# Performance work log

Hardware: AMD Instinct MI355X
Metric: run time of the kernel (lower is better)

Reference implementation:

```python
import jax, jax.numpy as jnp
import numpy as np

N, E, G, H = 100000, 1600000, 256, 2
EPS = 1e-5


def _gat_conv(x, src, dst, W, a_src, a_dst, bias, C):
    # PyG GATConv (concat=True, negative_slope=0.2): lin has no bias, bias added after concat.
    h = (x @ W).reshape(N, H, C)                                   # [N,H,C]
    e_src = (h * a_src).sum(-1)                                    # [N,H]
    e_dst = (h * a_dst).sum(-1)                                    # [N,H]
    alpha = jax.nn.leaky_relu(e_src[src] + e_dst[dst], 0.2)        # [Etot,H]
    amax = jax.ops.segment_max(alpha, dst, num_segments=N)         # segment softmax over incoming edges
    ex = jnp.exp(alpha - amax[dst])
    denom = jax.ops.segment_sum(ex, dst, num_segments=N)
    msg = h[src] * ex[:, :, None]                                  # [Etot,H,C]
    out = jax.ops.segment_sum(msg, dst, num_segments=N) / (denom[:, :, None] + 1e-16)
    return out.reshape(N, H * C) + bias


def _bn(x, g, b, m, v):  # BatchNorm in eval mode with running stats
    return g * (x - m) * jax.lax.rsqrt(v + EPS) + b


def _forward(edge_index, batch, x, w1, as1, ad1, b1, g1, be1, m1, v1, p1w, p1b,
             w2, as2, ad2, b2, g2, be2, m2, v2, p2w, p2b,
             w3, as3, ad3, b3, g3, be3, m3, v3, p3w, p3b,
             fw, fb, g4, be4, m4, v4, l1w, l1b, l2w, l2b):
    loops = jnp.arange(N, dtype=edge_index.dtype)                  # GATConv add_self_loops=True
    src = jnp.concatenate([edge_index[0], loops])
    dst = jnp.concatenate([edge_index[1], loops])
    h = jax.nn.relu(_bn(_gat_conv(x, src, dst, w1, as1, ad1, b1, 32), g1, be1, m1, v1)) + (x @ p1w + p1b)
    h = jax.nn.relu(_bn(_gat_conv(h, src, dst, w2, as2, ad2, b2, 64), g2, be2, m2, v2)) + (h @ p2w + p2b)
    h = jax.nn.relu(_bn(_gat_conv(h, src, dst, w3, as3, ad3, b3, 64), g3, be3, m3, v3)) + (h @ p3w + p3b)
    counts = jax.ops.segment_sum(jnp.ones((N,), h.dtype), batch, num_segments=G)
    pooled = jax.ops.segment_sum(h, batch, num_segments=G) / jnp.maximum(counts, 1.0)[:, None]  # [G,128]
    z = jax.nn.relu(_bn(pooled @ fw + fb, g4, be4, m4, v4))
    z = jax.nn.relu(z @ l1w + l1b)
    return z @ l2w + l2b                                           # [G,10]


def setup_inputs():
    key = jax.random.key(0)
    ks = jax.random.split(key, 48)
    it = iter(range(48))
    def rn(shape, s=0.1):
        return jax.random.normal(ks[next(it)], shape, jnp.float32) * s
    def bn_params(dim):  # gamma, beta, running_mean, running_var
        return (jax.random.uniform(ks[next(it)], (dim,), jnp.float32, 0.5, 1.5),
                rn((dim,)), rn((dim,)),
                jax.random.uniform(ks[next(it)], (dim,), jnp.float32, 0.5, 1.5))
    inp = {}
    inp["x"] = jax.random.normal(ks[next(it)], (N, 5), jnp.float32)
    inp["edge_index"] = jax.random.randint(ks[next(it)], (2, E), 0, N, jnp.int32)
    inp["batch"] = jnp.sort(jax.random.randint(ks[next(it)], (N,), 0, G, jnp.int32))
    inp["w1"], inp["as1"], inp["ad1"], inp["b1"] = rn((5, 64)), rn((H, 32)), rn((H, 32)), rn((64,))
    inp["g1"], inp["be1"], inp["m1"], inp["v1"] = bn_params(64)
    inp["p1w"], inp["p1b"] = rn((5, 64)), rn((64,))
    inp["w2"], inp["as2"], inp["ad2"], inp["b2"] = rn((64, 128)), rn((H, 64)), rn((H, 64)), rn((128,))
    inp["g2"], inp["be2"], inp["m2"], inp["v2"] = bn_params(128)
    inp["p2w"], inp["p2b"] = rn((64, 128)), rn((128,))
    inp["w3"], inp["as3"], inp["ad3"], inp["b3"] = rn((128, 128)), rn((H, 64)), rn((H, 64)), rn((128,))
    inp["g3"], inp["be3"], inp["m3"], inp["v3"] = bn_params(128)
    inp["p3w"], inp["p3b"] = rn((128, 128)), rn((128,))
    inp["fw"], inp["fb"] = rn((128, 32)), rn((32,))
    inp["g4"], inp["be4"], inp["m4"], inp["v4"] = bn_params(32)
    inp["l1w"], inp["l1b"] = rn((32, 32)), rn((32,))
    inp["l2w"], inp["l2b"] = rn((32, 10)), rn((10,))
    return inp


def reference(x, edge_index, batch, w1, as1, ad1, b1, g1, be1, m1, v1, p1w, p1b,
              w2, as2, ad2, b2, g2, be2, m2, v2, p2w, p2b,
              w3, as3, ad3, b3, g3, be3, m3, v3, p3w, p3b,
              fw, fb, g4, be4, m4, v4, l1w, l1b, l2w, l2b):
    return _forward(edge_index, batch, x, w1, as1, ad1, b1, g1, be1, m1, v1, p1w, p1b,
                    w2, as2, ad2, b2, g2, be2, m2, v2, p2w, p2b,
                    w3, as3, ad3, b3, g3, be3, m3, v3, p3w, p3b,
                    fw, fb, g4, be4, m4, v4, l1w, l1b, l2w, l2b)
```

## Files before the change

### kernel.cpp

```cpp
#include <hip/hip_runtime.h>
#include <hip/hip_bf16.h>
#include <hip/hip_fp16.h>

#define NN   100000
#define EE   1600000
#define ETOT (EE + NN)
#define GG   256
#define BNEPS 1e-5f
#define NBK  391
#define PADTOT (ETOT + NBK * 4096 + 64)
#define PSPLIT 16

typedef float floatx2 __attribute__((ext_vector_type(2)));
typedef short s16x8 __attribute__((ext_vector_type(8)));
typedef float f32x4v __attribute__((ext_vector_type(4)));

__device__ __forceinline__ unsigned short f2bf(float f) {
    unsigned u = __float_as_uint(f);
    unsigned r = u + 0x7FFF + ((u >> 16) & 1);
    return (unsigned short)(r >> 16);
}
__device__ __forceinline__ float bf2f(unsigned short b) {
    return __uint_as_float(((unsigned)b) << 16);
}
__device__ __forceinline__ floatx2 pkfma(floatx2 a, floatx2 b, floatx2 c) {
    return __builtin_elementwise_fma(a, b, c);
}


__global__ __launch_bounds__(256) void bucket_count_kernel(
    const int* __restrict__ ei, int* __restrict__ bucket_cnt)
{
    __shared__ int cnt[NBK];
    for (int i = threadIdx.x; i < NBK; i += 256) cnt[i] = 0;
    __syncthreads();
    int base = blockIdx.x * 8192;
    for (int k = threadIdx.x; k < 8192; k += 256) {
        int e = base + k;
        if (e < ETOT) {
            int dst = (e < EE) ? ei[EE + e] : (e - EE);
            atomicAdd(&cnt[dst >> 8], 1);
        }
    }
    __syncthreads();
    for (int i = threadIdx.x; i < NBK; i += 256)
        if (cnt[i]) atomicAdd(&bucket_cnt[i], cnt[i]);
}

__global__ __launch_bounds__(512) void bucket_scan_kernel(
    const int* __restrict__ bucket_cnt, int* __restrict__ bucket_base,
    int* __restrict__ gcursor, float* __restrict__ esrcs)
{
    __shared__ int s[512];
    int t = threadIdx.x;
    int v = (t < NBK) ? bucket_cnt[t] : 0;
    s[t] = v;
    __syncthreads();
    int x = v;
    for (int o = 1; o < 512; o <<= 1) {
        int y = (t >= o) ? s[t - o] : 0;
        __syncthreads();
        x += y;
        s[t] = x;
        __syncthreads();
    }
    if (t < NBK) { bucket_base[t] = x - v; gcursor[t] = x - v; }
    if (t == 0) {
        bucket_base[NBK] = ETOT;
        esrcs[2 * NN]     = __int_as_float(0xFF800000);
        esrcs[2 * NN + 1] = __int_as_float(0xFF800000);
    }
}

__global__ __launch_bounds__(256) void partition_kernel(
    const int* __restrict__ ei, int* __restrict__ gcursor, int* __restrict__ part)
{
    __shared__ int cnt[NBK];
    __shared__ int basel[NBK];
    for (int i = threadIdx.x; i < NBK; i += 256) cnt[i] = 0;
    __syncthreads();
    int base = blockIdx.x * 4096;
    for (int k = threadIdx.x; k < 4096; k += 256) {
        int e = base + k;
        if (e < ETOT) {
            int dst = (e < EE) ? ei[EE + e] : (e - EE);
            atomicAdd(&cnt[dst >> 8], 1);
        }
    }
    __syncthreads();
    for (int i = threadIdx.x; i < NBK; i += 256) {
        int c = cnt[i];
        basel[i] = c ? atomicAdd(&gcursor[i], c) : 0;
        cnt[i] = 0;
    }
    __syncthreads();
    for (int k = threadIdx.x; k < 4096; k += 256) {
        int e = base + k;
        if (e < ETOT) {
            int src, dst;
            if (e < EE) { src = ei[e]; dst = ei[EE + e]; }
            else        { src = e - EE; dst = e - EE; }
            int b = dst >> 8;
            int slot = atomicAdd(&cnt[b], 1);
            part[basel[b] + slot] = src | ((dst & 255) << 17);
        }
    }
}

__global__ __launch_bounds__(256) void csr_build_kernel(
    const int* __restrict__ part, const int* __restrict__ bucket_base,
    int* __restrict__ row2_start, int* __restrict__ row2_deg,
    int* __restrict__ csr2_src)
{
    __shared__ int degs[256];
    __shared__ int sc[256];
    __shared__ int cur[256];
    int b = blockIdx.x;
    int t = threadIdx.x;
    int beg = bucket_base[b], end = bucket_base[b + 1];
    int pbase = ((beg + 7) & ~7) + 4096 * b;
    degs[t] = 0;
    __syncthreads();
    for (int j = beg + t; j < end; j += 256)
        atomicAdd(&degs[(part[j] >> 17) & 255], 1);
    __syncthreads();
    int dg = degs[t];
    int pdeg = (dg + 7) & ~7;
    sc[t] = pdeg;
    __syncthreads();
    int x = pdeg;
    for (int o = 1; o < 256; o <<= 1) {
        int y = (t >= o) ? sc[t - o] : 0;
        __syncthreads();
        x += y;
        sc[t] = x;
        __syncthreads();
    }
    int start2 = pbase + (x - pdeg);
    int node = b * 256 + t;
    if (node < NN) { row2_start[node] = start2; row2_deg[node] = dg; }
    cur[t] = start2;
    __syncthreads();
    for (int j = beg + t; j < end; j += 256) {
        int pv = part[j];
        int pos = atomicAdd(&cur[(pv >> 17) & 255], 1);
        csr2_src[pos] = pv & 0x1FFFF;
    }
    for (int k = dg; k < pdeg; ++k) csr2_src[start2 + k] = NN;
}


template<int K>
__device__ __forceinline__ void prep_w_body(
    int unit, const float* __restrict__ W, const float* __restrict__ pw,
    short* __restrict__ wfrag)
{
    constexpr int KS = K / 32;
    int total = 16 * KS * 2 * 64;
    if (unit >= total) return;
    int lane = unit & 63;
    int rest = unit >> 6;
    int hilo = rest & 1;
    int fk = rest >> 1;
    int ks = fk % KS;
    int nt = fk / KS;
    int n = nt * 16 + (lane & 15);
    int k0 = ks * 32 + (lane >> 4) * 8;
    const float* src = (n < 128) ? (W + n) : (pw + (n - 128));
    s16x8 out;
#pragma unroll
    for (int j = 0; j < 8; ++j) {
        float wv = src[(size_t)(k0 + j) * 128];
        unsigned short hi = f2bf(wv);
        if (hilo == 0) {
            out[j] = (short)hi;
        } else {
            float fhi = __uint_as_float(((unsigned)hi) << 16);
            out[j] = (short)f2bf(wv - fhi);
        }
    }
    *(s16x8*)(wfrag + (size_t)unit * 8) = out;
}

__global__ __launch_bounds__(256) void prep_all_kernel(
    const float* __restrict__ w2, const float* __restrict__ p2w, short* __restrict__ wfrag2,
    const float* __restrict__ w3, const float* __restrict__ p3w, short* __restrict__ wfrag3,
    const float* b1, const float* g1, const float* be1, const float* m1, const float* v1,
    const float* b2, const float* g2, const float* be2, const float* m2, const float* v2,
    const float* b3, const float* g3, const float* be3, const float* m3, const float* v3,
    float* sc1, float* sh1, float* sc2, float* sh2, float* sc3, float* sh3)
{
    int b = blockIdx.x;
    int tid = threadIdx.x;
    if (b < 16) {
        prep_w_body<64>(b * 256 + tid, w2, p2w, wfrag2);
    } else if (b < 48) {
        prep_w_body<128>((b - 16) * 256 + tid, w3, p3w, wfrag3);
    } else {
        int t = tid;
        if (t < 128) {
            if (t < 64) {
                float sc = g1[t] * rsqrtf(v1[t] + BNEPS);
                sc1[t] = sc;
                sh1[t] = (b1[t] - m1[t]) * sc + be1[t];
            }
            {
                float sc = g2[t] * rsqrtf(v2[t] + BNEPS);
                sc2[t] = sc;
                sh2[t] = (b2[t] - m2[t]) * sc + be2[t];
            }
            {
                float sc = g3[t] * rsqrtf(v3[t] + BNEPS);
                sc3[t] = sc;
                sh3[t] = (b3[t] - m3[t]) * sc + be3[t];
            }
        }
    }
}


__global__ __launch_bounds__(256) void edgew_kernel(
    const int* __restrict__ csr2_src, const int* __restrict__ row2_start,
    const int* __restrict__ row2_deg,
    const float2* __restrict__ esrc, const float2* __restrict__ edst,
    unsigned* __restrict__ csr_w, int nN)
{
    int n = blockIdx.x * 8 + (threadIdx.x >> 5);
    int hl = threadIdx.x & 31;
    if (n >= nN) return;
    float2 ed = edst[n];
    int s2 = row2_start[n];
    int dg = row2_deg[n];
    int pc = (dg + 7) & ~7;
    for (int j = hl; j < pc; j += 32) {
        int i = csr2_src[s2 + j];
        float2 es = esrc[i];
        float a0 = es.x + ed.x; a0 = (a0 > 0.f) ? a0 : 0.2f * a0;
        float a1 = es.y + ed.y; a1 = (a1 > 0.f) ? a1 : 0.2f * a1;
        unsigned w = (unsigned)f2bf(__expf(a0)) | ((unsigned)f2bf(__expf(a1)) << 16);
        csr_w[s2 + j] = w;
    }
}


__global__ __launch_bounds__(256) void feat1_kernel(
    const float* __restrict__ xin, const float* __restrict__ W,
    const float* __restrict__ pw, const float* __restrict__ pb,
    const float* __restrict__ a_src, const float* __restrict__ a_dst,
    unsigned char* __restrict__ h8, float* __restrict__ esrc, float* __restrict__ edst,
    unsigned short* __restrict__ rout16, int nN)
{
    constexpr int F_IN = 5, F_OUT = 64;
    int t = threadIdx.x;
    int n = blockIdx.x * 4 + t / F_OUT;
    int f = t % F_OUT;
    if (n >= nN) return;
    float acc = 0.f, racc = 0.f;
#pragma unroll
    for (int k = 0; k < F_IN; ++k) {
        float xv = xin[n * F_IN + k];
        acc  += xv * W[k * F_OUT + f];
        racc += xv * pw[k * F_OUT + f];
    }
    float other = __shfl_xor(acc, 1, 64);
    if ((f & 1) == 0) {
        int p = __builtin_amdgcn_cvt_pk_fp8_f32(acc, other, 0, false);
        *(unsigned short*)(h8 + (size_t)n * F_OUT + f) = (unsigned short)(p & 0xFFFF);
    }
    rout16[(size_t)n * F_OUT + f] = f2bf(racc + pb[f]);
    float es = acc * a_src[f];
    float ed = acc * a_dst[f];
#pragma unroll
    for (int off = 16; off > 0; off >>= 1) {
        es += __shfl_xor(es, off, 32);
        ed += __shfl_xor(ed, off, 32);
    }
    if ((t & 31) == 0) {
        int head = (f >> 5) & 1;
        esrc[n * 2 + head] = es;
        edst[n * 2 + head] = ed;
    }
}


template<int K>
__global__ __launch_bounds__(512, 4) void mfma_feat_kernel(
    const unsigned short* __restrict__ xin16, const short* __restrict__ wfrag,
    const float* __restrict__ pb,
    const float* __restrict__ a_src, const float* __restrict__ a_dst,
    unsigned char* __restrict__ h8, float* __restrict__ esrc, float* __restrict__ edst,
    unsigned short* __restrict__ rout16)
{
    constexpr int KS = K / 32;
    constexpr int CH = K / 8;
    __shared__ __align__(16) char smem[1024 * CH + 28672];
    s16x8* xs = (s16x8*)smem;
    unsigned short* h8lds = (unsigned short*)(smem + 1024 * CH);
    unsigned short* rolds = (unsigned short*)(smem + 1024 * CH + 9216);
    float2* espart = (float2*)(smem + 1024 * CH + 26624);

    const int tid = threadIdx.x;
    const int base = blockIdx.x * 64;

    for (int idx = tid; idx < 64 * CH; idx += 512) {
        int node = idx / CH;
        int ch = idx % CH;
        int gn = base + node; if (gn > NN - 1) gn = NN - 1;
        s16x8 v = *(const s16x8*)(xin16 + (size_t)gn * K + ch * 8);
        int tt = node >> 4, mm = node & 15;
        xs[(tt * CH + ch) * 16 + mm] = v;
    }
    __syncthreads();

    const int w = tid >> 6;
    const int lane = tid & 63;
    const int quad = lane >> 4;
    const int m = lane & 15;
    const int nt0 = 2 * w, nt1 = nt0 + 1;

    s16x8 bA[2 * KS], bB[2 * KS];
#pragma unroll
    for (int i = 0; i < 2 * KS; ++i) {
        bA[i] = *(const s16x8*)(wfrag + (size_t)((nt0 * KS * 2 + i) * 64 + lane) * 8);
        bB[i] = *(const s16x8*)(wfrag + (size_t)((nt1 * KS * 2 + i) * 64 + lane) * 8);
    }

    const bool hpart = (w < 4);
    float av0 = 0.f, dv0 = 0.f, av1 = 0.f, dv1 = 0.f, bv0 = 0.f, bv1 = 0.f;
    if (hpart) {
        av0 = a_src[nt0 * 16 + m]; dv0 = a_dst[nt0 * 16 + m];
        av1 = a_src[nt1 * 16 + m]; dv1 = a_dst[nt1 * 16 + m];
    } else {
        bv0 = pb[(nt0 - 8) * 16 + m]; bv1 = pb[(nt1 - 8) * 16 + m];
    }

#pragma unroll
    for (int rt = 0; rt < 4; ++rt) {
        s16x8 a[KS];
#pragma unroll
        for (int ks = 0; ks < KS; ++ks)
            a[ks] = xs[(rt * CH + ks * 4 + quad) * 16 + m];
        f32x4v cA = {0.f, 0.f, 0.f, 0.f};
        f32x4v cB = {0.f, 0.f, 0.f, 0.f};
#pragma unroll
        for (int ks = 0; ks < KS; ++ks) {
            cA = __builtin_amdgcn_mfma_f32_16x16x32_bf16(a[ks], bA[2 * ks + 0], cA, 0, 0, 0);
            cA = __builtin_amdgcn_mfma_f32_16x16x32_bf16(a[ks], bA[2 * ks + 1], cA, 0, 0, 0);
            cB = __builtin_amdgcn_mfma_f32_16x16x32_bf16(a[ks], bB[2 * ks + 0], cB, 0, 0, 0);
            cB = __builtin_amdgcn_mfma_f32_16x16x32_bf16(a[ks], bB[2 * ks + 1], cB, 0, 0, 0);
        }
        int row0 = rt * 16 + quad * 4;
        if (hpart) {
#pragma unroll
            for (int r = 0; r < 4; ++r) {
                float v0 = cA[r], v1 = cB[r];
                float es = v0 * av0 + v1 * av1;
                float ed = v0 * dv0 + v1 * dv1;
#pragma unroll
                for (int off = 8; off > 0; off >>= 1) {
                    es += __shfl_xor(es, off, 16);
                    ed += __shfl_xor(ed, off, 16);
                }
                if (m == 0) espart[w * 64 + row0 + r] = make_float2(es, ed);
                float p0 = __shfl_xor(v0, 1, 16);
                float p1 = __shfl_xor(v1, 1, 16);
                if ((m & 1) == 0) {
                    int pk0 = __builtin_amdgcn_cvt_pk_fp8_f32(v0, p0, 0, false);
                    int pk1 = __builtin_amdgcn_cvt_pk_fp8_f32(v1, p1, 0, false);
                    h8lds[(row0 + r) * 72 + nt0 * 8 + (m >> 1)] = (unsigned short)(pk0 & 0xFFFF);
                    h8lds[(row0 + r) * 72 + nt1 * 8 + (m >> 1)] = (unsigned short)(pk1 & 0xFFFF);
                }
            }
        } else {
#pragma unroll
            for (int r = 0; r < 4; ++r) {
                rolds[(row0 + r) * 136 + (nt0 - 8) * 16 + m] = f2bf(cA[r] + bv0);
                rolds[(row0 + r) * 136 + (nt1 - 8) * 16 + m] = f2bf(cB[r] + bv1);
            }
        }
    }

    __syncthreads();

    if (tid < 64) {
        int node = base + tid;
        if (node < NN) {
            float2 e0 = espart[0 * 64 + tid];
            float2 e1 = espart[1 * 64 + tid];
            float2 e2 = espart[2 * 64 + tid];
            float2 e3 = espart[3 * 64 + tid];
            ((float2*)esrc)[node] = make_float2(e0.x + e1.x, e2.x + e3.x);
            ((float2*)edst)[node] = make_float2(e0.y + e1.y, e2.y + e3.y);
        }
    }
    for (int i = tid; i < 64 * 8; i += 512) {
        int row = i >> 3, ch = i & 7;
        int node = base + row;
        if (node < NN) {
            int4 v = *(const int4*)((char*)h8lds + row * 144 + ch * 16);
            *(int4*)(h8 + (size_t)node * 128 + ch * 16) = v;
        }
    }
    for (int i = tid; i < 64 * 16; i += 512) {
        int row = i >> 4, ch = i & 15;
        int node = base + row;
        if (node < NN) {
            int4 v = *(const int4*)((char*)rolds + row * 272 + ch * 16);
            *(int4*)((char*)rout16 + (size_t)node * 256 + ch * 16) = v;
        }
    }
}


__global__ __launch_bounds__(256) void aggregate128_kernel(
    const unsigned char* __restrict__ h8,
    const int* __restrict__ row2_start, const int* __restrict__ row2_deg,
    const int* __restrict__ csr2_src, const unsigned* __restrict__ csr_w,
    const float* __restrict__ bnsc, const float* __restrict__ bnsh,
    unsigned short* __restrict__ io16)
{
    int w = threadIdx.x >> 6;
    int lane = threadIdx.x & 63;
    int half = lane >> 5;
    int fl = lane & 31;
    unsigned shl = (fl >= 16) ? 0u : 16u;
    int n = blockIdx.x * 8 + w * 2 + half;
    int s2 = row2_start[n];
    int dg = row2_deg[n];
    int pc = (dg + 7) & ~7;
    const int4* sp = (const int4*)(csr2_src + s2);
    const uint4* wp = (const uint4*)(csr_w + s2);
    float sa = 0.f, sb = 0.f;
    floatx2 acc01a = {0.f, 0.f}, acc23a = {0.f, 0.f};
    floatx2 acc01b = {0.f, 0.f}, acc23b = {0.f, 0.f};
    for (int j = 0; j < pc; j += 8) {
        int4 ia = sp[(j >> 2) + 0];
        int4 ib = sp[(j >> 2) + 1];
        uint4 wa = wp[(j >> 2) + 0];
        uint4 wb = wp[(j >> 2) + 1];
        unsigned d0 = *(const unsigned*)(h8 + (size_t)ia.x * 128 + fl * 4);
        unsigned d1 = *(const unsigned*)(h8 + (size_t)ia.y * 128 + fl * 4);
        unsigned d2 = *(const unsigned*)(h8 + (size_t)ia.z * 128 + fl * 4);
        unsigned d3 = *(const unsigned*)(h8 + (size_t)ia.w * 128 + fl * 4);
        unsigned d4 = *(const unsigned*)(h8 + (size_t)ib.x * 128 + fl * 4);
        unsigned d5 = *(const unsigned*)(h8 + (size_t)ib.y * 128 + fl * 4);
        unsigned d6 = *(const unsigned*)(h8 + (size_t)ib.z * 128 + fl * 4);
        unsigned d7 = *(const unsigned*)(h8 + (size_t)ib.w * 128 + fl * 4);
        float g0 = __uint_as_float((wa.x << shl) & 0xFFFF0000u);
        float g1 = __uint_as_float((wa.y << shl) & 0xFFFF0000u);
        float g2 = __uint_as_float((wa.z << shl) & 0xFFFF0000u);
        float g3 = __uint_as_float((wa.w << shl) & 0xFFFF0000u);
        float g4 = __uint_as_float((wb.x << shl) & 0xFFFF0000u);
        float g5 = __uint_as_float((wb.y << shl) & 0xFFFF0000u);
        float g6 = __uint_as_float((wb.z << shl) & 0xFFFF0000u);
        float g7 = __uint_as_float((wb.w << shl) & 0xFFFF0000u);
        floatx2 gv0 = {g0, g0};
        floatx2 gv1 = {g1, g1};
        floatx2 gv2 = {g2, g2};
        floatx2 gv3 = {g3, g3};
        floatx2 gv4 = {g4, g4};
        floatx2 gv5 = {g5, g5};
        floatx2 gv6 = {g6, g6};
        floatx2 gv7 = {g7, g7};
        acc01a = pkfma(gv0, __builtin_amdgcn_cvt_pk_f32_fp8((int)d0, false), acc01a);
        acc23a = pkfma(gv0, __builtin_amdgcn_cvt_pk_f32_fp8((int)d0, true),  acc23a);
        acc01a = pkfma(gv1, __builtin_amdgcn_cvt_pk_f32_fp8((int)d1, false), acc01a);
        acc23a = pkfma(gv1, __builtin_amdgcn_cvt_pk_f32_fp8((int)d1, true),  acc23a);
        acc01a = pkfma(gv2, __builtin_amdgcn_cvt_pk_f32_fp8((int)d2, false), acc01a);
        acc23a = pkfma(gv2, __builtin_amdgcn_cvt_pk_f32_fp8((int)d2, true),  acc23a);
        acc01a = pkfma(gv3, __builtin_amdgcn_cvt_pk_f32_fp8((int)d3, false), acc01a);
        acc23a = pkfma(gv3, __builtin_amdgcn_cvt_pk_f32_fp8((int)d3, true),  acc23a);
        acc01b = pkfma(gv4, __builtin_amdgcn_cvt_pk_f32_fp8((int)d4, false), acc01b);
        acc23b = pkfma(gv4, __builtin_amdgcn_cvt_pk_f32_fp8((int)d4, true),  acc23b);
        acc01b = pkfma(gv5, __builtin_amdgcn_cvt_pk_f32_fp8((int)d5, false), acc01b);
        acc23b = pkfma(gv5, __builtin_amdgcn_cvt_pk_f32_fp8((int)d5, true),  acc23b);
        acc01b = pkfma(gv6, __builtin_amdgcn_cvt_pk_f32_fp8((int)d6, false), acc01b);
        acc23b = pkfma(gv6, __builtin_amdgcn_cvt_pk_f32_fp8((int)d6, true),  acc23b);
        acc01b = pkfma(gv7, __builtin_amdgcn_cvt_pk_f32_fp8((int)d7, false), acc01b);
        acc23b = pkfma(gv7, __builtin_amdgcn_cvt_pk_f32_fp8((int)d7, true),  acc23b);
        sa += ((g0 + g1) + (g2 + g3));
        sb += ((g4 + g5) + (g6 + g7));
    }
    floatx2 acc01 = acc01a + acc01b;
    floatx2 acc23 = acc23a + acc23b;
    float s = sa + sb;
    float inv = 1.f / (s + 1e-16f);
    int f0 = fl * 4;
    float4 sc = *(const float4*)(bnsc + f0);
    float4 sh = *(const float4*)(bnsh + f0);
    float o0 = fmaf(acc01.x * inv, sc.x, sh.x);
    float o1 = fmaf(acc01.y * inv, sc.y, sh.y);
    float o2 = fmaf(acc23.x * inv, sc.z, sh.z);
    float o3 = fmaf(acc23.y * inv, sc.w, sh.w);
    uint2* iop = (uint2*)(io16 + (size_t)n * 128 + f0);
    uint2 pu = *iop;
    float r0 = fmaxf(o0, 0.f) + __uint_as_float((pu.x & 0xFFFFu) << 16);
    float r1 = fmaxf(o1, 0.f) + __uint_as_float(pu.x & 0xFFFF0000u);
    float r2 = fmaxf(o2, 0.f) + __uint_as_float((pu.y & 0xFFFFu) << 16);
    float r3 = fmaxf(o3, 0.f) + __uint_as_float(pu.y & 0xFFFF0000u);
    uint2 ov;
    ov.x = (unsigned)f2bf(r0) | ((unsigned)f2bf(r1) << 16);
    ov.y = (unsigned)f2bf(r2) | ((unsigned)f2bf(r3) << 16);
    *iop = ov;
}


__global__ __launch_bounds__(256) void aggregate64_kernel(
    const unsigned char* __restrict__ h8,
    const int* __restrict__ row2_start, const int* __restrict__ row2_deg,
    const int* __restrict__ csr2_src, const unsigned* __restrict__ csr_w,
    const float* __restrict__ bnsc, const float* __restrict__ bnsh,
    unsigned short* __restrict__ io16)
{
    int w = threadIdx.x >> 6;
    int lane = threadIdx.x & 63;
    int half = lane >> 5;
    int hl = lane & 31;
    int q  = hl >> 4;
    int fl = hl & 15;
    unsigned shl = (fl >= 8) ? 0u : 16u;
    int n = blockIdx.x * 8 + w * 2 + half;
    int s2 = row2_start[n];
    int dg = row2_deg[n];
    int pc = (dg + 7) & ~7;
    const int4* sp = (const int4*)(csr2_src + s2);
    const uint4* wp = (const uint4*)(csr_w + s2);
    float s = 0.f;
    floatx2 acc01 = {0.f, 0.f}, acc23 = {0.f, 0.f};
    for (int j = 0; j < pc; j += 8) {
        int4 ia = sp[(j >> 2) + 0];
        int4 ib = sp[(j >> 2) + 1];
        uint4 wa = wp[(j >> 2) + 0];
        uint4 wb = wp[(j >> 2) + 1];
        int i0 = q ? ia.y : ia.x;
        int i1 = q ? ia.w : ia.z;
        int i2 = q ? ib.y : ib.x;
        int i3 = q ? ib.w : ib.z;
        unsigned w0 = q ? wa.y : wa.x;
        unsigned w1 = q ? wa.w : wa.z;
        unsigned w2 = q ? wb.y : wb.x;
        unsigned w3 = q ? wb.w : wb.z;
        unsigned d0 = *(const unsigned*)(h8 + (size_t)i0 * 64 + fl * 4);
        unsigned d1 = *(const unsigned*)(h8 + (size_t)i1 * 64 + fl * 4);
        unsigned d2 = *(const unsigned*)(h8 + (size_t)i2 * 64 + fl * 4);
        unsigned d3 = *(const unsigned*)(h8 + (size_t)i3 * 64 + fl * 4);
        float g0 = __uint_as_float((w0 << shl) & 0xFFFF0000u);
        float g1 = __uint_as_float((w1 << shl) & 0xFFFF0000u);
        float g2 = __uint_as_float((w2 << shl) & 0xFFFF0000u);
        float g3 = __uint_as_float((w3 << shl) & 0xFFFF0000u);
        floatx2 gv0 = {g0, g0};
        floatx2 gv1 = {g1, g1};
        floatx2 gv2 = {g2, g2};
        floatx2 gv3 = {g3, g3};
        acc01 = pkfma(gv0, __builtin_amdgcn_cvt_pk_f32_fp8((int)d0, false), acc01);
        acc23 = pkfma(gv0, __builtin_amdgcn_cvt_pk_f32_fp8((int)d0, true),  acc23);
        acc01 = pkfma(gv1, __builtin_amdgcn_cvt_pk_f32_fp8((int)d1, false), acc01);
        acc23 = pkfma(gv1, __builtin_amdgcn_cvt_pk_f32_fp8((int)d1, true),  acc23);
        acc01 = pkfma(gv2, __builtin_amdgcn_cvt_pk_f32_fp8((int)d2, false), acc01);
        acc23 = pkfma(gv2, __builtin_amdgcn_cvt_pk_f32_fp8((int)d2, true),  acc23);
        acc01 = pkfma(gv3, __builtin_amdgcn_cvt_pk_f32_fp8((int)d3, false), acc01);
        acc23 = pkfma(gv3, __builtin_amdgcn_cvt_pk_f32_fp8((int)d3, true),  acc23);
        s += ((g0 + g1) + (g2 + g3));
    }
    acc01.x += __shfl_xor(acc01.x, 16);
    acc01.y += __shfl_xor(acc01.y, 16);
    acc23.x += __shfl_xor(acc23.x, 16);
    acc23.y += __shfl_xor(acc23.y, 16);
    s += __shfl_xor(s, 16);
    if (hl < 16) {
        float inv = 1.f / (s + 1e-16f);
        int f0 = fl * 4;
        float4 sc = *(const float4*)(bnsc + f0);
        float4 sh = *(const float4*)(bnsh + f0);
        float o0 = fmaf(acc01.x * inv, sc.x, sh.x);
        float o1 = fmaf(acc01.y * inv, sc.y, sh.y);
        float o2 = fmaf(acc23.x * inv, sc.z, sh.z);
        float o3 = fmaf(acc23.y * inv, sc.w, sh.w);
        uint2* iop = (uint2*)(io16 + (size_t)n * 64 + f0);
        uint2 pu = *iop;
        float r0 = fmaxf(o0, 0.f) + __uint_as_float((pu.x & 0xFFFFu) << 16);
        float r1 = fmaxf(o1, 0.f) + __uint_as_float(pu.x & 0xFFFF0000u);
        float r2 = fmaxf(o2, 0.f) + __uint_as_float((pu.y & 0xFFFFu) << 16);
        float r3 = fmaxf(o3, 0.f) + __uint_as_float(pu.y & 0xFFFF0000u);
        uint2 ov;
        ov.x = (unsigned)f2bf(r0) | ((unsigned)f2bf(r1) << 16);
        ov.y = (unsigned)f2bf(r2) | ((unsigned)f2bf(r3) << 16);
        *iop = ov;
    }
}


__global__ __launch_bounds__(128) void pool_partial_kernel(
    const unsigned short* __restrict__ hf16, const int* __restrict__ batch,
    float* __restrict__ ppart)
{
    int g = blockIdx.x / PSPLIT;
    int p = blockIdx.x % PSPLIT;
    int f = threadIdx.x;
    int lo = 0, hi = NN;
    while (lo < hi) { int mid = (lo + hi) >> 1; if (batch[mid] < g) lo = mid + 1; else hi = mid; }
    int start = lo;
    hi = NN;
    while (lo < hi) { int mid = (lo + hi) >> 1; if (batch[mid] < g + 1) lo = mid + 1; else hi = mid; }
    int end = lo;
    int len = end - start;
    int chunk = (len + PSPLIT - 1) / PSPLIT;
    int i0 = start + p * chunk;
    int i1 = i0 + chunk; if (i1 > end) i1 = end;
    float acc = 0.f;
    for (int i = i0; i < i1; ++i) acc += bf2f(hf16[(size_t)i * 128 + f]);
    ppart[((size_t)g * PSPLIT + p) * 128 + f] = acc;
}


__global__ __launch_bounds__(128) void head_kernel(
    const float* __restrict__ ppart, const int* __restrict__ batch,
    const float* __restrict__ fw, const float* __restrict__ fb,
    const float* __restrict__ g4, const float* __restrict__ be4,
    const float* __restrict__ m4, const float* __restrict__ v4,
    const float* __restrict__ l1w, const float* __restrict__ l1b,
    const float* __restrict__ l2w, const float* __restrict__ l2b,
    float* __restrict__ out)
{
    __shared__ float p[128];
    __shared__ float z1[32];
    __shared__ float z2[32];
    int g = blockIdx.x, t = threadIdx.x;
    int lo = 0, hi = NN;
    while (lo < hi) { int mid = (lo + hi) >> 1; if (batch[mid] < g) lo = mid + 1; else hi = mid; }
    int start = lo;
    hi = NN;
    while (lo < hi) { int mid = (lo + hi) >> 1; if (batch[mid] < g + 1) lo = mid + 1; else hi = mid; }
    float cnt = (float)(lo - start);
    float acc = 0.f;
#pragma unroll
    for (int q = 0; q < PSPLIT; ++q)
        acc += ppart[((size_t)g * PSPLIT + q) * 128 + t];
    p[t] = acc / fmaxf(cnt, 1.0f);
    __syncthreads();
    if (t < 32) {
        float a = fb[t];
        for (int k = 0; k < 128; ++k) a += p[k] * fw[k * 32 + t];
        float val = g4[t] * (a - m4[t]) * rsqrtf(v4[t] + BNEPS) + be4[t];
        z1[t] = fmaxf(val, 0.f);
    }
    __syncthreads();
    if (t < 32) {
        float a = l1b[t];
        for (int k = 0; k < 32; ++k) a += z1[k] * l1w[k * 32 + t];
        z2[t] = fmaxf(a, 0.f);
    }
    __syncthreads();
    if (t < 10) {
        float a = l2b[t];
        for (int k = 0; k < 32; ++k) a += z2[k] * l2w[k * 10 + t];
        out[g * 10 + t] = a;
    }
}


extern "C" void kernel_launch(void* const* d_in, const int* in_sizes, int n_in,
                              void* d_out, int out_size, void* d_ws, size_t ws_size,
                              hipStream_t stream) {
    const float* x     = (const float*)d_in[0];
    const int*   ei    = (const int*)d_in[1];
    const int*   batch = (const int*)d_in[2];
    const float* w1  = (const float*)d_in[3];
    const float* as1 = (const float*)d_in[4];
    const float* ad1 = (const float*)d_in[5];
    const float* b1  = (const float*)d_in[6];
    const float* g1  = (const float*)d_in[7];
    const float* be1 = (const float*)d_in[8];
    const float* m1  = (const float*)d_in[9];
    const float* v1  = (const float*)d_in[10];
    const float* p1w = (const float*)d_in[11];
    const float* p1b = (const float*)d_in[12];
    const float* w2  = (const float*)d_in[13];
    const float* as2 = (const float*)d_in[14];
    const float* ad2 = (const float*)d_in[15];
    const float* b2  = (const float*)d_in[16];
    const float* g2  = (const float*)d_in[17];
    const float* be2 = (const float*)d_in[18];
    const float* m2  = (const float*)d_in[19];
    const float* v2  = (const float*)d_in[20];
    const float* p2w = (const float*)d_in[21];
    const float* p2b = (const float*)d_in[22];
    const float* w3  = (const float*)d_in[23];
    const float* as3 = (const float*)d_in[24];
    const float* ad3 = (const float*)d_in[25];
    const float* b3  = (const float*)d_in[26];
    const float* g3  = (const float*)d_in[27];
    const float* be3 = (const float*)d_in[28];
    const float* m3  = (const float*)d_in[29];
    const float* v3  = (const float*)d_in[30];
    const float* p3w = (const float*)d_in[31];
    const float* p3b = (const float*)d_in[32];
    const float* fw  = (const float*)d_in[33];
    const float* fb  = (const float*)d_in[34];
    const float* g4  = (const float*)d_in[35];
    const float* be4 = (const float*)d_in[36];
    const float* m4  = (const float*)d_in[37];
    const float* v4  = (const float*)d_in[38];
    const float* l1w = (const float*)d_in[39];
    const float* l1b = (const float*)d_in[40];
    const float* l2w = (const float*)d_in[41];
    const float* l2b = (const float*)d_in[42];

    char* ws = (char*)d_ws;
    size_t off = 0;
    auto alloc = [&](size_t bytes) -> char* {
        char* p = ws + off;
        off += (bytes + 255) & ~(size_t)255;
        return p;
    };
    int*    bucket_cnt  = (int*)alloc((NBK) * sizeof(int));
    int*    bucket_base = (int*)alloc((NBK + 1) * sizeof(int));
    int*    gcursor     = (int*)alloc((NBK) * sizeof(int));
    int*    part        = (int*)alloc((size_t)ETOT * sizeof(int));
    int*    row2_start  = (int*)alloc(NN * sizeof(int));
    int*    row2_deg    = (int*)alloc(NN * sizeof(int));
    int*    csr2_src    = (int*)alloc((size_t)PADTOT * sizeof(int));
    unsigned* csr_w     = (unsigned*)alloc((size_t)PADTOT * sizeof(unsigned));
    unsigned char*  h8  = (unsigned char*)alloc((size_t)(NN + 1) * 128);
    unsigned short* hb1 = (unsigned short*)alloc((size_t)NN * 64 * sizeof(short));
    unsigned short* hb2 = (unsigned short*)alloc((size_t)NN * 128 * sizeof(short));
    unsigned short* hb3 = (unsigned short*)alloc((size_t)NN * 128 * sizeof(short));
    float*  esrc        = (float*)alloc((size_t)(NN + 1) * 2 * sizeof(float));
    float*  edst        = (float*)alloc((size_t)NN * 2 * sizeof(float));
    float*  ppart       = (float*)alloc((size_t)GG * PSPLIT * 128 * sizeof(float));
    short*  wfrag2      = (short*)alloc((size_t)16 * 2 * 2 * 64 * 8 * sizeof(short));
    short*  wfrag3      = (short*)alloc((size_t)16 * 4 * 2 * 64 * 8 * sizeof(short));
    float*  bnsc1       = (float*)alloc(64 * sizeof(float));
    float*  bnsh1       = (float*)alloc(64 * sizeof(float));
    float*  bnsc2       = (float*)alloc(128 * sizeof(float));
    float*  bnsh2       = (float*)alloc(128 * sizeof(float));
    float*  bnsc3       = (float*)alloc(128 * sizeof(float));
    float*  bnsh3       = (float*)alloc(128 * sizeof(float));

    prep_all_kernel<<<49, 256, 0, stream>>>(
        w2, p2w, wfrag2, w3, p3w, wfrag3,
        b1, g1, be1, m1, v1, b2, g2, be2, m2, v2, b3, g3, be3, m3, v3,
        bnsc1, bnsh1, bnsc2, bnsh2, bnsc3, bnsh3);

    hipMemsetAsync(bucket_cnt, 0, NBK * sizeof(int), stream);
    bucket_count_kernel<<<(ETOT + 8191) / 8192, 256, 0, stream>>>(ei, bucket_cnt);
    bucket_scan_kernel<<<1, 512, 0, stream>>>(bucket_cnt, bucket_base, gcursor, esrc);
    partition_kernel<<<(ETOT + 4095) / 4096, 256, 0, stream>>>(ei, gcursor, part);
    csr_build_kernel<<<NBK, 256, 0, stream>>>(part, bucket_base, row2_start, row2_deg, csr2_src);

    feat1_kernel<<<(NN + 3) / 4, 256, 0, stream>>>(
        x, w1, p1w, p1b, as1, ad1, h8, esrc, edst, hb1, NN);
    edgew_kernel<<<(NN + 7) / 8, 256, 0, stream>>>(
        csr2_src, row2_start, row2_deg, (const float2*)esrc, (const float2*)edst, csr_w, NN);
    aggregate64_kernel<<<NN / 8, 256, 0, stream>>>(
        h8, row2_start, row2_deg, csr2_src, csr_w, bnsc1, bnsh1, hb1);

    mfma_feat_kernel<64><<<(NN + 63) / 64, 512, 0, stream>>>(
        hb1, wfrag2, p2b, as2, ad2, h8, esrc, edst, hb2);
    edgew_kernel<<<(NN + 7) / 8, 256, 0, stream>>>(
        csr2_src, row2_start, row2_deg, (const float2*)esrc, (const float2*)edst, csr_w, NN);
    aggregate128_kernel<<<NN / 8, 256, 0, stream>>>(
        h8, row2_start, row2_deg, csr2_src, csr_w, bnsc2, bnsh2, hb2);

    mfma_feat_kernel<128><<<(NN + 63) / 64, 512, 0, stream>>>(
        hb2, wfrag3, p3b, as3, ad3, h8, esrc, edst, hb3);
    edgew_kernel<<<(NN + 7) / 8, 256, 0, stream>>>(
        csr2_src, row2_start, row2_deg, (const float2*)esrc, (const float2*)edst, csr_w, NN);
    aggregate128_kernel<<<NN / 8, 256, 0, stream>>>(
        h8, row2_start, row2_deg, csr2_src, csr_w, bnsc3, bnsh3, hb3);

    pool_partial_kernel<<<GG * PSPLIT, 128, 0, stream>>>(hb3, batch, ppart);
    head_kernel<<<GG, 128, 0, stream>>>(ppart, batch, fw, fb, g4, be4, m4, v4,
                                        l1w, l1b, l2w, l2b, (float*)d_out);
}
```

Before: 471.3 us.

## Fuse edge attention weight computation into aggregation kernels

Removes the separate edgew kernel that computed per-edge exp(leaky_relu) weights into a csr_w buffer. Each aggregation kernel now computes these weights in-lane from esrc/edst and broadcasts them across lanes with shuffles. This drops three launches and the write/read round trip of about 1.7M weights per layer. In exchange it adds a gather of esrc, an exp and eight shuffles per 8-edge chunk inside the aggregation loop, and keeps the weights in fp32 instead of bf16.

```diff
diff --git a/kernel.cpp b/kernel.cpp
--- a/kernel.cpp
+++ b/kernel.cpp
@@ -219,30 +219,6 @@
 }
 
 
-__global__ __launch_bounds__(256) void edgew_kernel(
-    const int* __restrict__ csr2_src, const int* __restrict__ row2_start,
-    const int* __restrict__ row2_deg,
-    const float2* __restrict__ esrc, const float2* __restrict__ edst,
-    unsigned* __restrict__ csr_w, int nN)
-{
-    int n = blockIdx.x * 8 + (threadIdx.x >> 5);
-    int hl = threadIdx.x & 31;
-    if (n >= nN) return;
-    float2 ed = edst[n];
-    int s2 = row2_start[n];
-    int dg = row2_deg[n];
-    int pc = (dg + 7) & ~7;
-    for (int j = hl; j < pc; j += 32) {
-        int i = csr2_src[s2 + j];
-        float2 es = esrc[i];
-        float a0 = es.x + ed.x; a0 = (a0 > 0.f) ? a0 : 0.2f * a0;
-        float a1 = es.y + ed.y; a1 = (a1 > 0.f) ? a1 : 0.2f * a1;
-        unsigned w = (unsigned)f2bf(__expf(a0)) | ((unsigned)f2bf(__expf(a1)) << 16);
-        csr_w[s2 + j] = w;
-    }
-}
-
-
 __global__ __launch_bounds__(256) void feat1_kernel(
     const float* __restrict__ xin, const float* __restrict__ W,
     const float* __restrict__ pw, const float* __restrict__ pb,
@@ -415,29 +391,52 @@
 __global__ __launch_bounds__(256) void aggregate128_kernel(
     const unsigned char* __restrict__ h8,
     const int* __restrict__ row2_start, const int* __restrict__ row2_deg,
-    const int* __restrict__ csr2_src, const unsigned* __restrict__ csr_w,
+    const int* __restrict__ csr2_src,
+    const float* __restrict__ esrc, const float2* __restrict__ edst,
     const float* __restrict__ bnsc, const float* __restrict__ bnsh,
     unsigned short* __restrict__ io16)
 {
     int w = threadIdx.x >> 6;
     int lane = threadIdx.x & 63;
     int half = lane >> 5;
-    int fl = lane & 31;
-    unsigned shl = (fl >= 16) ? 0u : 16u;
+    int hl = lane & 31;
+    int fl = hl;
+    bool headhi = fl >= 16;
+    int e = hl & 7;
+    int chead = (hl >> 3) & 1;
+    int bsrc = half * 32 + (headhi ? 8 : 0);
     int n = blockIdx.x * 8 + w * 2 + half;
+    float2 edv = edst[n];
+    float edh = chead ? edv.y : edv.x;
     int s2 = row2_start[n];
     int dg = row2_deg[n];
     int pc = (dg + 7) & ~7;
     const int4* sp = (const int4*)(csr2_src + s2);
-    const uint4* wp = (const uint4*)(csr_w + s2);
-    float sa = 0.f, sb = 0.f;
+    float s = 0.f;
     floatx2 acc01a = {0.f, 0.f}, acc23a = {0.f, 0.f};
     floatx2 acc01b = {0.f, 0.f}, acc23b = {0.f, 0.f};
     for (int j = 0; j < pc; j += 8) {
         int4 ia = sp[(j >> 2) + 0];
         int4 ib = sp[(j >> 2) + 1];
-        uint4 wa = wp[(j >> 2) + 0];
-        uint4 wb = wp[(j >> 2) + 1];
+        int cx = (e & 4) ? ib.x : ia.x;
+        int cy = (e & 4) ? ib.y : ia.y;
+        int cz = (e & 4) ? ib.z : ia.z;
+        int cw = (e & 4) ? ib.w : ia.w;
+        int cxy = (e & 1) ? cy : cx;
+        int czw = (e & 1) ? cw : cz;
+        int ie = (e & 2) ? czw : cxy;
+        float esv = esrc[(size_t)ie * 2 + chead];
+        float av = esv + edh;
+        av = (av > 0.f) ? av : 0.2f * av;
+        float g = __expf(av);
+        float g0 = __shfl(g, bsrc + 0, 64);
+        float g1 = __shfl(g, bsrc + 1, 64);
+        float g2 = __shfl(g, bsrc + 2, 64);
+        float g3 = __shfl(g, bsrc + 3, 64);
+        float g4 = __shfl(g, bsrc + 4, 64);
+        float g5 = __shfl(g, bsrc + 5, 64);
+        float g6 = __shfl(g, bsrc + 6, 64);
+        float g7 = __shfl(g, bsrc + 7, 64);
         unsigned d0 = *(const unsigned*)(h8 + (size_t)ia.x * 128 + fl * 4);
         unsigned d1 = *(const unsigned*)(h8 + (size_t)ia.y * 128 + fl * 4);
         unsigned d2 = *(const unsigned*)(h8 + (size_t)ia.z * 128 + fl * 4);
@@ -446,14 +445,6 @@
         unsigned d5 = *(const unsigned*)(h8 + (size_t)ib.y * 128 + fl * 4);
         unsigned d6 = *(const unsigned*)(h8 + (size_t)ib.z * 128 + fl * 4);
         unsigned d7 = *(const unsigned*)(h8 + (size_t)ib.w * 128 + fl * 4);
-        float g0 = __uint_as_float((wa.x << shl) & 0xFFFF0000u);
-        float g1 = __uint_as_float((wa.y << shl) & 0xFFFF0000u);
-        float g2 = __uint_as_float((wa.z << shl) & 0xFFFF0000u);
-        float g3 = __uint_as_float((wa.w << shl) & 0xFFFF0000u);
-        float g4 = __uint_as_float((wb.x << shl) & 0xFFFF0000u);
-        float g5 = __uint_as_float((wb.y << shl) & 0xFFFF0000u);
-        float g6 = __uint_as_float((wb.z << shl) & 0xFFFF0000u);
-        float g7 = __uint_as_float((wb.w << shl) & 0xFFFF0000u);
         floatx2 gv0 = {g0, g0};
         floatx2 gv1 = {g1, g1};
         floatx2 gv2 = {g2, g2};
@@ -478,12 +469,10 @@
         acc23b = pkfma(gv6, __builtin_amdgcn_cvt_pk_f32_fp8((int)d6, true),  acc23b);
         acc01b = pkfma(gv7, __builtin_amdgcn_cvt_pk_f32_fp8((int)d7, false), acc01b);
         acc23b = pkfma(gv7, __builtin_amdgcn_cvt_pk_f32_fp8((int)d7, true),  acc23b);
-        sa += ((g0 + g1) + (g2 + g3));
-        sb += ((g4 + g5) + (g6 + g7));
+        s += (((g0 + g1) + (g2 + g3)) + ((g4 + g5) + (g6 + g7)));
     }
     floatx2 acc01 = acc01a + acc01b;
     floatx2 acc23 = acc23a + acc23b;
-    float s = sa + sb;
     float inv = 1.f / (s + 1e-16f);
     int f0 = fl * 4;
     float4 sc = *(const float4*)(bnsc + f0);
@@ -508,7 +497,8 @@
 __global__ __launch_bounds__(256) void aggregate64_kernel(
     const unsigned char* __restrict__ h8,
     const int* __restrict__ row2_start, const int* __restrict__ row2_deg,
-    const int* __restrict__ csr2_src, const unsigned* __restrict__ csr_w,
+    const int* __restrict__ csr2_src,
+    const float* __restrict__ esrc, const float2* __restrict__ edst,
     const float* __restrict__ bnsc, const float* __restrict__ bnsh,
     unsigned short* __restrict__ io16)
 {
@@ -518,36 +508,45 @@
     int hl = lane & 31;
     int q  = hl >> 4;
     int fl = hl & 15;
-    unsigned shl = (fl >= 8) ? 0u : 16u;
+    bool headhi = fl >= 8;
+    int e = hl & 7;
+    int chead = (hl >> 3) & 1;
+    int bsrc = half * 32 + (headhi ? 8 : 0);
     int n = blockIdx.x * 8 + w * 2 + half;
+    float2 edv = edst[n];
+    float edh = chead ? edv.y : edv.x;
     int s2 = row2_start[n];
     int dg = row2_deg[n];
     int pc = (dg + 7) & ~7;
     const int4* sp = (const int4*)(csr2_src + s2);
-    const uint4* wp = (const uint4*)(csr_w + s2);
     float s = 0.f;
     floatx2 acc01 = {0.f, 0.f}, acc23 = {0.f, 0.f};
     for (int j = 0; j < pc; j += 8) {
         int4 ia = sp[(j >> 2) + 0];
         int4 ib = sp[(j >> 2) + 1];
-        uint4 wa = wp[(j >> 2) + 0];
-        uint4 wb = wp[(j >> 2) + 1];
+        int cx = (e & 4) ? ib.x : ia.x;
+        int cy = (e & 4) ? ib.y : ia.y;
+        int cz = (e & 4) ? ib.z : ia.z;
+        int cw = (e & 4) ? ib.w : ia.w;
+        int cxy = (e & 1) ? cy : cx;
+        int czw = (e & 1) ? cw : cz;
+        int iec = (e & 2) ? czw : cxy;
+        float esv = esrc[(size_t)iec * 2 + chead];
+        float av = esv + edh;
+        av = (av > 0.f) ? av : 0.2f * av;
+        float g = __expf(av);
+        float g0 = __shfl(g, bsrc + q, 64);
+        float g1 = __shfl(g, bsrc + 2 + q, 64);
+        float g2 = __shfl(g, bsrc + 4 + q, 64);
+        float g3 = __shfl(g, bsrc + 6 + q, 64);
         int i0 = q ? ia.y : ia.x;
         int i1 = q ? ia.w : ia.z;
         int i2 = q ? ib.y : ib.x;
         int i3 = q ? ib.w : ib.z;
-        unsigned w0 = q ? wa.y : wa.x;
-        unsigned w1 = q ? wa.w : wa.z;
-        unsigned w2 = q ? wb.y : wb.x;
-        unsigned w3 = q ? wb.w : wb.z;
         unsigned d0 = *(const unsigned*)(h8 + (size_t)i0 * 64 + fl * 4);
         unsigned d1 = *(const unsigned*)(h8 + (size_t)i1 * 64 + fl * 4);
         unsigned d2 = *(const unsigned*)(h8 + (size_t)i2 * 64 + fl * 4);
         unsigned d3 = *(const unsigned*)(h8 + (size_t)i3 * 64 + fl * 4);
-        float g0 = __uint_as_float((w0 << shl) & 0xFFFF0000u);
-        float g1 = __uint_as_float((w1 << shl) & 0xFFFF0000u);
-        float g2 = __uint_as_float((w2 << shl) & 0xFFFF0000u);
-        float g3 = __uint_as_float((w3 << shl) & 0xFFFF0000u);
         floatx2 gv0 = {g0, g0};
         floatx2 gv1 = {g1, g1};
         floatx2 gv2 = {g2, g2};
@@ -720,7 +719,6 @@
     int*    row2_start  = (int*)alloc(NN * sizeof(int));
     int*    row2_deg    = (int*)alloc(NN * sizeof(int));
     int*    csr2_src    = (int*)alloc((size_t)PADTOT * sizeof(int));
-    unsigned* csr_w     = (unsigned*)alloc((size_t)PADTOT * sizeof(unsigned));
     unsigned char*  h8  = (unsigned char*)alloc((size_t)(NN + 1) * 128);
     unsigned short* hb1 = (unsigned short*)alloc((size_t)NN * 64 * sizeof(short));
     unsigned short* hb2 = (unsigned short*)alloc((size_t)NN * 128 * sizeof(short));
@@ -750,24 +748,18 @@
 
     feat1_kernel<<<(NN + 3) / 4, 256, 0, stream>>>(
         x, w1, p1w, p1b, as1, ad1, h8, esrc, edst, hb1, NN);
-    edgew_kernel<<<(NN + 7) / 8, 256, 0, stream>>>(
-        csr2_src, row2_start, row2_deg, (const float2*)esrc, (const float2*)edst, csr_w, NN);
     aggregate64_kernel<<<NN / 8, 256, 0, stream>>>(
-        h8, row2_start, row2_deg, csr2_src, csr_w, bnsc1, bnsh1, hb1);
+        h8, row2_start, row2_deg, csr2_src, esrc, (const float2*)edst, bnsc1, bnsh1, hb1);
 
     mfma_feat_kernel<64><<<(NN + 63) / 64, 512, 0, stream>>>(
         hb1, wfrag2, p2b, as2, ad2, h8, esrc, edst, hb2);
-    edgew_kernel<<<(NN + 7) / 8, 256, 0, stream>>>(
-        csr2_src, row2_start, row2_deg, (const float2*)esrc, (const float2*)edst, csr_w, NN);
     aggregate128_kernel<<<NN / 8, 256, 0, stream>>>(
-        h8, row2_start, row2_deg, csr2_src, csr_w, bnsc2, bnsh2, hb2);
+        h8, row2_start, row2_deg, csr2_src, esrc, (const float2*)edst, bnsc2, bnsh2, hb2);
 
     mfma_feat_kernel<128><<<(NN + 63) / 64, 512, 0, stream>>>(
         hb2, wfrag3, p3b, as3, ad3, h8, esrc, edst, hb3);
-    edgew_kernel<<<(NN + 7) / 8, 256, 0, stream>>>(
-        csr2_src, row2_start, row2_deg, (const float2*)esrc, (const float2*)edst, csr_w, NN);
     aggregate128_kernel<<<NN / 8, 256, 0, stream>>>(
-        h8, row2_start, row2_deg, csr2_src, csr_w, bnsc3, bnsh3, hb3);
+        h8, row2_start, row2_deg, csr2_src, esrc, (const float2*)edst, bnsc3, bnsh3, hb3);
 
     pool_partial_kernel<<<GG * PSPLIT, 128, 0, stream>>>(hb3, batch, ppart);
     head_kernel<<<GG, 128, 0, stream>>>(ppart, batch, fw, fb, g4, be4, m4, v4,
```

After: 433.6 us, median of 2. 8.0% less time.
